# Kernel tuning notes

Hardware: AMD Instinct MI355X
Metric: run time of the kernel (lower is better)

The kernel has to match this reference:

```python
import jax, jax.numpy as jnp
import numpy as np

TEMPERATURE = 0.1

# Constant linear map replacing the nested-loop diagonal masks:
# M[i, j, k] = 1 if i + j == k, shape (10, 10, 19).
_ii, _jj = np.meshgrid(np.arange(10), np.arange(10), indexing='ij')
_M = np.zeros((10, 10, 19), dtype=np.float32)
_M[_ii, _jj, _ii + _jj] = 1.0
DIAG_SUM = jnp.asarray(_M)


def setup_inputs() -> dict:
    key = jax.random.key(0)
    ks = jax.random.split(key, 8)
    B = 16384
    grid = jax.random.normal(ks[0], (B, 4, 28, 28), dtype=jnp.float32)
    # random one-hot program ids
    pid = jax.random.randint(ks[1], (B,), 0, 4)
    program_onehot = jax.nn.one_hot(pid, 4, dtype=jnp.float32)
    W1 = jax.random.normal(ks[2], (784, 256), dtype=jnp.float32) * 0.05
    b1 = jnp.zeros((256,), dtype=jnp.float32)
    W2 = jax.random.normal(ks[3], (256, 10), dtype=jnp.float32) * 0.05
    b2 = jnp.zeros((10,), dtype=jnp.float32)
    Wp = jax.random.normal(ks[4], (4, 16), dtype=jnp.float32) * 0.3
    bp = jnp.zeros((16,), dtype=jnp.float32)
    Wr1 = jax.random.normal(ks[5], (16, 4), dtype=jnp.float32) * 0.3
    br1 = jnp.zeros((4,), dtype=jnp.float32)
    Wr2 = jax.random.normal(ks[6], (16, 4), dtype=jnp.float32) * 0.3
    br2 = jnp.zeros((4,), dtype=jnp.float32)
    return {"grid": grid, "program_onehot": program_onehot,
            "W1": W1, "b1": b1, "W2": W2, "b2": b2,
            "Wp": Wp, "bp": bp, "Wr1": Wr1, "br1": br1,
            "Wr2": Wr2, "br2": br2}


def reference(grid, program_onehot, W1, b1, W2, b2, Wp, bp, Wr1, br1, Wr2, br2):
    B = grid.shape[0]
    # digit_net: 784 -> 256 -> 10 MLP on each of the 4 sub-images
    x = grid.reshape(B * 4, 784)
    h1 = jax.nn.relu(x @ W1 + b1)
    logits = h1 @ W2 + b2                       # (B*4, 10)
    digit_probs = jax.nn.softmax(logits / TEMPERATURE, axis=-1).reshape(B, 4, 10)
    # pointer network
    h = program_onehot @ Wp + bp                 # (B, 16)
    ptr1 = jax.nn.softmax(h @ Wr1 + br1, axis=-1)  # (B, 4)
    ptr2 = jax.nn.softmax(h @ Wr2 + br2, axis=-1)  # (B, 4)
    dist1 = jnp.einsum('bp,bpd->bd', ptr1, digit_probs)  # (B, 10)
    dist2 = jnp.einsum('bp,bpd->bd', ptr2, digit_probs)  # (B, 10)
    outer = dist1[:, :, None] * dist2[:, None, :]         # (B, 10, 10)
    outer_sym = 0.5 * (outer + jnp.swapaxes(outer, 1, 2))
    # diagonal-sum convolution as one contraction against the constant map
    sum_distribution = jnp.einsum('bij,ijk->bk', outer_sym, DIAG_SUM)  # (B, 19)
    return jnp.log(sum_distribution + 1e-10)
```

## Files before the change

### kernel.cpp

```cpp
#include <hip/hip_runtime.h>
#include <hip/hip_bf16.h>

typedef __attribute__((ext_vector_type(8))) short bf16x8;
typedef __attribute__((ext_vector_type(4))) float f32x4;

__device__ __forceinline__ short f2bf(float f) {
    union { float f; unsigned u; } v; v.f = f;
    unsigned r = v.u + 0x7fffu + ((v.u >> 16) & 1u);
    return (short)(r >> 16);
}

#define KP  800
#define LDK 40
#define NKT 25

__global__ void init_kernel(const float* __restrict__ W1, const float* __restrict__ W2,
                            const float* __restrict__ Wp, const float* __restrict__ bp,
                            const float* __restrict__ Wr1, const float* __restrict__ br1,
                            const float* __restrict__ Wr2, const float* __restrict__ br2,
                            short* __restrict__ w1t, short* __restrict__ w2t,
                            float* __restrict__ ptabs)
{
    int tid = blockIdx.x * blockDim.x + threadIdx.x;
    int stride = gridDim.x * blockDim.x;
    for (int i = tid; i < 256 * KP; i += stride) {
        int n = i / KP, k = i - n * KP;
        float v = (k < 784) ? W1[k * 256 + n] : 0.f;
        w1t[i] = f2bf(v);
    }
    for (int i = tid; i < 16 * 256; i += stride) {
        int n = i >> 8, k = i & 255;
        float v = (n < 10) ? W2[k * 10 + n] : 0.f;
        w2t[i] = f2bf(v);
    }
    if (blockIdx.x == 0 && threadIdx.x < 8) {
        int which = threadIdx.x >> 2, p = threadIdx.x & 3;
        const float* Wr = which ? Wr2 : Wr1;
        const float* br = which ? br2 : br1;
        float s[4];
        for (int q = 0; q < 4; q++) {
            float a = br[q];
            for (int j = 0; j < 16; j++) a += (Wp[p * 16 + j] + bp[j]) * Wr[j * 4 + q];
            s[q] = a;
        }
        float m = fmaxf(fmaxf(s[0], s[1]), fmaxf(s[2], s[3]));
        float e[4]; float tot = 0.f;
        for (int q = 0; q < 4; q++) { e[q] = __expf(s[q] - m); tot += e[q]; }
        for (int q = 0; q < 4; q++) ptabs[which * 16 + p * 4 + q] = e[q] / tot;
    }
}

__global__ __launch_bounds__(512, 4) void fused_kernel(
    const float* __restrict__ g_in, const float* __restrict__ onehot,
    const float* __restrict__ b1g, const float* __restrict__ b2g,
    const short* __restrict__ w1t, const short* __restrict__ w2t,
    const float* __restrict__ ptabs, float* __restrict__ out)
{
    __shared__ __align__(16) char lds[78464];
    short* Abuf = (short*)lds;
    short* Bbuf = (short*)(lds + 20480);
    short* h1   = (short*)lds;
    float* probs = (float*)(lds + 67584);
    float* dist1 = (float*)(lds + 75776);
    float* dist2 = (float*)(lds + 77056);

    const int t = threadIdx.x;
    const int lane = t & 63, wave = t >> 6;
    const int l16 = lane & 15, lg = lane >> 4;
    const int wr = wave >> 2, wc = wave & 3;
    const int blk = blockIdx.x;

    const int ar = t >> 2, aq = t & 3;
    const int bn = t >> 1, bh = t & 1;
    const float* gA = g_in + ((long)blk * 128 + ar) * 784 + aq * 8;
    const short* gB = w1t + bn * KP + bh * 16;
    short* awp = Abuf + ar * LDK + aq * 8;
    short* bwp = Bbuf + bn * LDK + bh * 16;

    f32x4 acc[4][4];
    #pragma unroll
    for (int mi = 0; mi < 4; mi++)
        #pragma unroll
        for (int ni = 0; ni < 4; ni++)
            acc[mi][ni] = (f32x4)0.f;

    f32x4 x0, x1; bf16x8 y0, y1;
    auto load_tile = [&](int kt) {
        const int k0 = kt * 32;
        if (k0 + aq * 8 < 784) {
            x0 = *(const f32x4*)(gA + k0);
            x1 = *(const f32x4*)(gA + k0 + 4);
        } else { x0 = (f32x4)0.f; x1 = (f32x4)0.f; }
        y0 = *(const bf16x8*)(gB + k0);
        y1 = *(const bf16x8*)(gB + k0 + 8);
    };
    auto write_tile = [&](int buf) {
        bf16x8 a8;
        a8[0] = f2bf(x0[0]); a8[1] = f2bf(x0[1]); a8[2] = f2bf(x0[2]); a8[3] = f2bf(x0[3]);
        a8[4] = f2bf(x1[0]); a8[5] = f2bf(x1[1]); a8[6] = f2bf(x1[2]); a8[7] = f2bf(x1[3]);
        *(bf16x8*)(awp + buf * (128 * LDK)) = a8;
        *(bf16x8*)(bwp + buf * (256 * LDK)) = y0;
        *(bf16x8*)(bwp + buf * (256 * LDK) + 8) = y1;
    };

    load_tile(0); write_tile(0);
    __syncthreads();
    int cur = 0;
    for (int kt = 0; kt < NKT; kt++) {
        const bool more = (kt + 1 < NKT);
        if (more) load_tile(kt + 1);
        const short* ab = Abuf + cur * (128 * LDK);
        const short* bb = Bbuf + cur * (256 * LDK);
        bf16x8 aF[4], bF[4];
        #pragma unroll
        for (int mi = 0; mi < 4; mi++)
            aF[mi] = *(const bf16x8*)(ab + (wr * 64 + mi * 16 + l16) * LDK + lg * 8);
        #pragma unroll
        for (int ni = 0; ni < 4; ni++)
            bF[ni] = *(const bf16x8*)(bb + (wc * 64 + ni * 16 + l16) * LDK + lg * 8);
        #pragma unroll
        for (int mi = 0; mi < 4; mi++)
            #pragma unroll
            for (int ni = 0; ni < 4; ni++)
                acc[mi][ni] = __builtin_amdgcn_mfma_f32_16x16x32_bf16(aF[mi], bF[ni], acc[mi][ni], 0, 0, 0);
        if (more) write_tile(cur ^ 1);
        __syncthreads();
        cur ^= 1;
    }

    #pragma unroll
    for (int mi = 0; mi < 4; mi++) {
        const int R = wr * 64 + mi * 16 + lg * 4;
        #pragma unroll
        for (int ni = 0; ni < 4; ni++) {
            const int N = wc * 64 + ni * 16 + l16;
            const float bias = b1g[N];
            #pragma unroll
            for (int j = 0; j < 4; j++) {
                float v = acc[mi][ni][j] + bias;
                h1[(R + j) * 264 + N] = f2bf(fmaxf(v, 0.f));
            }
        }
    }
    __syncthreads();

    f32x4 acc2 = (f32x4)0.f;
    const short* h1r = h1 + (wave * 16 + l16) * 264 + lg * 8;
    const short* w2r = w2t + l16 * 256 + lg * 8;
    #pragma unroll
    for (int kk = 0; kk < 8; kk++) {
        bf16x8 a2 = *(const bf16x8*)(h1r + kk * 32);
        bf16x8 b2f = *(const bf16x8*)(w2r + kk * 32);
        acc2 = __builtin_amdgcn_mfma_f32_16x16x32_bf16(a2, b2f, acc2, 0, 0, 0);
    }

    const float b2v = (l16 < 10) ? b2g[l16] : 0.f;
    float pv[4], mx[4];
    #pragma unroll
    for (int j = 0; j < 4; j++) {
        pv[j] = (l16 < 10) ? (acc2[j] + b2v) * 10.f : -1e30f;
        mx[j] = pv[j];
    }
    #pragma unroll
    for (int off = 1; off < 16; off <<= 1)
        #pragma unroll
        for (int j = 0; j < 4; j++)
            mx[j] = fmaxf(mx[j], __shfl_xor(mx[j], off));
    float ex[4], sm[4];
    #pragma unroll
    for (int j = 0; j < 4; j++) { ex[j] = __expf(pv[j] - mx[j]); sm[j] = ex[j]; }
    #pragma unroll
    for (int off = 1; off < 16; off <<= 1)
        #pragma unroll
        for (int j = 0; j < 4; j++)
            sm[j] += __shfl_xor(sm[j], off);
    #pragma unroll
    for (int j = 0; j < 4; j++)
        probs[(wave * 16 + lg * 4 + j) * 16 + l16] = ex[j] / sm[j];
    __syncthreads();

    if (t < 320) {
        int s = t / 10, d = t - s * 10;
        const float* oh = onehot + ((long)blk * 32 + s) * 4;
        int pid = (int)(oh[1] + 2.f * oh[2] + 3.f * oh[3] + 0.5f);
        const float* p1t = ptabs + pid * 4;
        const float* p2t = ptabs + 16 + pid * 4;
        float d1 = 0.f, d2 = 0.f;
        #pragma unroll
        for (int p = 0; p < 4; p++) {
            float pr = probs[(s * 4 + p) * 16 + d];
            d1 += p1t[p] * pr;
            d2 += p2t[p] * pr;
        }
        dist1[s * 10 + d] = d1;
        dist2[s * 10 + d] = d2;
    }
    __syncthreads();

    for (int idx = t; idx < 608; idx += 512) {
        int s = idx / 19, k = idx - s * 19;
        int ilo = k > 9 ? k - 9 : 0;
        int ihi = k < 9 ? k : 9;
        float sum = 0.f;
        for (int i = ilo; i <= ihi; i++)
            sum += dist1[s * 10 + i] * dist2[s * 10 + (k - i)];
        out[((long)blk * 32 + s) * 19 + k] = __logf(sum + 1e-10f);
    }
}

extern "C" void kernel_launch(void* const* d_in, const int* in_sizes, int n_in,
                              void* d_out, int out_size, void* d_ws, size_t ws_size,
                              hipStream_t stream)
{
    const float* grid   = (const float*)d_in[0];
    const float* onehot = (const float*)d_in[1];
    const float* W1  = (const float*)d_in[2];
    const float* b1  = (const float*)d_in[3];
    const float* W2  = (const float*)d_in[4];
    const float* b2  = (const float*)d_in[5];
    const float* Wp  = (const float*)d_in[6];
    const float* bp  = (const float*)d_in[7];
    const float* Wr1 = (const float*)d_in[8];
    const float* br1 = (const float*)d_in[9];
    const float* Wr2 = (const float*)d_in[10];
    const float* br2 = (const float*)d_in[11];
    float* out = (float*)d_out;

    short* w1t = (short*)d_ws;
    short* w2t = w1t + 256 * KP;
    float* ptabs = (float*)(w2t + 16 * 256);

    init_kernel<<<256, 256, 0, stream>>>(W1, W2, Wp, bp, Wr1, br1, Wr2, br2, w1t, w2t, ptabs);

    const int B = in_sizes[1] / 4;
    const int nblk = (B * 4) / 128;
    fused_kernel<<<nblk, 512, 0, stream>>>(grid, onehot, b1, b2, w1t, w2t, ptabs, out);
}
```

Before: 55.91 us.

## Load W1 tiles directly into LDS and deepen the A-operand prefetch pipeline

The W1 operand tiles are now copied straight from global memory into LDS with global_load_lds, so they no longer pass through registers and ds_write. The A (grid) tiles are prefetched two K-steps ahead, using manually unrolled ping-pong buffers with explicit vmcnt/lgkmcnt waits and raw s_barrier. The init kernel now reads W1 in coalesced order when transposing it. In exchange, the B tile in LDS loses its padding (row stride 32), which can cause bank conflicts on fragment reads, and the hand-placed waitcnt values must stay correct.

```diff
diff --git a/kernel.cpp b/kernel.cpp
--- a/kernel.cpp
+++ b/kernel.cpp
@@ -10,9 +10,22 @@
     return (short)(r >> 16);
 }
 
+__device__ __forceinline__ void gl2lds16(const void* g, void* l) {
+    __builtin_amdgcn_global_load_lds(
+        (const __attribute__((address_space(1))) unsigned int*)g,
+        (__attribute__((address_space(3))) unsigned int*)l,
+        16, 0, 0);
+}
+
 #define KP  800
-#define LDK 40
 #define NKT 25
+#define LDKA 40
+
+#define WAITV2 asm volatile("s_waitcnt vmcnt(2)" ::: "memory")
+#define WAITV0 asm volatile("s_waitcnt vmcnt(0)" ::: "memory")
+#define WAITL  asm volatile("s_waitcnt lgkmcnt(0)" ::: "memory")
+#define SBAR   __builtin_amdgcn_s_barrier()
+#define SCHED0 __builtin_amdgcn_sched_barrier(0)
 
 __global__ void init_kernel(const float* __restrict__ W1, const float* __restrict__ W2,
                             const float* __restrict__ Wp, const float* __restrict__ bp,
@@ -23,10 +36,13 @@
 {
     int tid = blockIdx.x * blockDim.x + threadIdx.x;
     int stride = gridDim.x * blockDim.x;
-    for (int i = tid; i < 256 * KP; i += stride) {
-        int n = i / KP, k = i - n * KP;
-        float v = (k < 784) ? W1[k * 256 + n] : 0.f;
-        w1t[i] = f2bf(v);
+    for (int i = tid; i < 784 * 256; i += stride) {
+        int k = i >> 8, n = i & 255;
+        w1t[n * KP + k] = f2bf(W1[i]);
+    }
+    for (int i = tid; i < 256 * 16; i += stride) {
+        int n = i >> 4, k = 784 + (i & 15);
+        w1t[n * KP + k] = 0;
     }
     for (int i = tid; i < 16 * 256; i += stride) {
         int n = i >> 8, k = i & 255;
@@ -71,11 +87,9 @@
     const int blk = blockIdx.x;
 
     const int ar = t >> 2, aq = t & 3;
-    const int bn = t >> 1, bh = t & 1;
     const float* gA = g_in + ((long)blk * 128 + ar) * 784 + aq * 8;
-    const short* gB = w1t + bn * KP + bh * 16;
-    short* awp = Abuf + ar * LDK + aq * 8;
-    short* bwp = Bbuf + bn * LDK + bh * 16;
+    const short* gB = w1t + ar * KP + aq * 8;
+    char* lB = (char*)Bbuf + wave * 1024;
 
     f32x4 acc[4][4];
     #pragma unroll
@@ -84,49 +98,76 @@
         for (int ni = 0; ni < 4; ni++)
             acc[mi][ni] = (f32x4)0.f;
 
-    f32x4 x0, x1; bf16x8 y0, y1;
-    auto load_tile = [&](int kt) {
+    f32x4 xa0, xa1, xb0, xb1;
+
+    auto issueA = [&](int kt, f32x4& x0, f32x4& x1) {
         const int k0 = kt * 32;
         if (k0 + aq * 8 < 784) {
             x0 = *(const f32x4*)(gA + k0);
             x1 = *(const f32x4*)(gA + k0 + 4);
         } else { x0 = (f32x4)0.f; x1 = (f32x4)0.f; }
-        y0 = *(const bf16x8*)(gB + k0);
-        y1 = *(const bf16x8*)(gB + k0 + 8);
-    };
-    auto write_tile = [&](int buf) {
+    };
+    auto issueB = [&](int kt, int buf) {
+        const short* g0 = gB + kt * 32;
+        char* l0 = lB + buf * 16384;
+        gl2lds16(g0, l0);
+        gl2lds16(g0 + 128 * KP, l0 + 8192);
+    };
+    auto writeA = [&](const f32x4& x0, const f32x4& x1, int buf) {
         bf16x8 a8;
         a8[0] = f2bf(x0[0]); a8[1] = f2bf(x0[1]); a8[2] = f2bf(x0[2]); a8[3] = f2bf(x0[3]);
         a8[4] = f2bf(x1[0]); a8[5] = f2bf(x1[1]); a8[6] = f2bf(x1[2]); a8[7] = f2bf(x1[3]);
-        *(bf16x8*)(awp + buf * (128 * LDK)) = a8;
-        *(bf16x8*)(bwp + buf * (256 * LDK)) = y0;
-        *(bf16x8*)(bwp + buf * (256 * LDK) + 8) = y1;
-    };
-
-    load_tile(0); write_tile(0);
-    __syncthreads();
-    int cur = 0;
-    for (int kt = 0; kt < NKT; kt++) {
-        const bool more = (kt + 1 < NKT);
-        if (more) load_tile(kt + 1);
-        const short* ab = Abuf + cur * (128 * LDK);
-        const short* bb = Bbuf + cur * (256 * LDK);
+        *(bf16x8*)(Abuf + buf * (128 * LDKA) + ar * LDKA + aq * 8) = a8;
+    };
+    auto mfmaStep = [&](int buf) {
+        const short* ab = Abuf + buf * (128 * LDKA);
+        const short* bb = Bbuf + buf * (256 * 32);
         bf16x8 aF[4], bF[4];
         #pragma unroll
         for (int mi = 0; mi < 4; mi++)
-            aF[mi] = *(const bf16x8*)(ab + (wr * 64 + mi * 16 + l16) * LDK + lg * 8);
+            aF[mi] = *(const bf16x8*)(ab + (wr * 64 + mi * 16 + l16) * LDKA + lg * 8);
         #pragma unroll
         for (int ni = 0; ni < 4; ni++)
-            bF[ni] = *(const bf16x8*)(bb + (wc * 64 + ni * 16 + l16) * LDK + lg * 8);
+            bF[ni] = *(const bf16x8*)(bb + (wc * 64 + ni * 16 + l16) * 32 + lg * 8);
         #pragma unroll
         for (int mi = 0; mi < 4; mi++)
             #pragma unroll
             for (int ni = 0; ni < 4; ni++)
                 acc[mi][ni] = __builtin_amdgcn_mfma_f32_16x16x32_bf16(aF[mi], bF[ni], acc[mi][ni], 0, 0, 0);
-        if (more) write_tile(cur ^ 1);
-        __syncthreads();
-        cur ^= 1;
-    }
+    };
+
+    issueB(0, 0); SCHED0;
+    issueA(0, xa0, xa1); SCHED0;
+    issueA(1, xb0, xb1); SCHED0;
+    writeA(xa0, xa1, 0);
+    WAITV2; WAITL; SBAR;
+
+    for (int it = 0; it < 11; ++it) {
+        const int kt = it * 2;
+        issueB(kt + 1, 1); SCHED0;
+        issueA(kt + 2, xa0, xa1); SCHED0;
+        mfmaStep(0);
+        writeA(xb0, xb1, 1);
+        WAITV2; WAITL; SBAR;
+        issueB(kt + 2, 0); SCHED0;
+        issueA(kt + 3, xb0, xb1); SCHED0;
+        mfmaStep(1);
+        writeA(xa0, xa1, 0);
+        WAITV2; WAITL; SBAR;
+    }
+    issueB(23, 1); SCHED0;
+    issueA(24, xa0, xa1); SCHED0;
+    mfmaStep(0);
+    writeA(xb0, xb1, 1);
+    WAITV2; WAITL; SBAR;
+
+    issueB(24, 0); SCHED0;
+    mfmaStep(1);
+    writeA(xa0, xa1, 0);
+    WAITV0; WAITL; SBAR;
+
+    mfmaStep(0);
+    WAITL; SBAR;
 
     #pragma unroll
     for (int mi = 0; mi < 4; mi++) {
```

New measurement: 56.82 us. No clear change (+1.6%).

## Halve M tile to 64 rows and restructure GEMM pipeline with decoupled A/B staging

Applied to the files above, without the earlier changes.

Each block now handles 64 rows instead of 128, doubling the grid. The A operand is staged in 128-wide K chunks and the B operand in 32-wide chunks, each double-buffered. The main loop is hand-unrolled with explicit lgkmcnt waits and raw barriers, and init_kernel now reads W1 coalesced when transposing it. The aim is better occupancy and overlap of global loads with MFMA, at the cost of reloading W1 twice as often across blocks, and it relies on hand-placed barriers being correct.

```diff
diff --git a/kernel.cpp b/kernel.cpp
--- a/kernel.cpp
+++ b/kernel.cpp
@@ -10,9 +10,15 @@
     return (short)(r >> 16);
 }
 
-#define KP  800
-#define LDK 40
-#define NKT 25
+#define KP    896
+#define KSTEP 128
+#define LDA   136
+#define LDB   40
+#define ABUFS (64 * LDA)
+#define BBUFS (256 * LDB)
+
+#define WAITL  asm volatile("s_waitcnt lgkmcnt(0)" ::: "memory")
+#define SBAR   __builtin_amdgcn_s_barrier()
 
 __global__ void init_kernel(const float* __restrict__ W1, const float* __restrict__ W2,
                             const float* __restrict__ Wp, const float* __restrict__ bp,
@@ -23,10 +29,13 @@
 {
     int tid = blockIdx.x * blockDim.x + threadIdx.x;
     int stride = gridDim.x * blockDim.x;
-    for (int i = tid; i < 256 * KP; i += stride) {
-        int n = i / KP, k = i - n * KP;
-        float v = (k < 784) ? W1[k * 256 + n] : 0.f;
-        w1t[i] = f2bf(v);
+    for (int i = tid; i < 784 * 256; i += stride) {
+        int k = i >> 8, n = i & 255;
+        w1t[n * KP + k] = f2bf(W1[i]);
+    }
+    for (int i = tid; i < 256 * 112; i += stride) {
+        int n = i / 112, k = 784 + (i % 112);
+        w1t[n * KP + k] = 0;
     }
     for (int i = tid; i < 16 * 256; i += stride) {
         int n = i >> 8, k = i & 255;
@@ -56,13 +65,13 @@
     const short* __restrict__ w1t, const short* __restrict__ w2t,
     const float* __restrict__ ptabs, float* __restrict__ out)
 {
-    __shared__ __align__(16) char lds[78464];
+    __shared__ __align__(16) char lds[79616];
     short* Abuf = (short*)lds;
-    short* Bbuf = (short*)(lds + 20480);
+    short* Bbuf = (short*)(lds + 34816);
     short* h1   = (short*)lds;
-    float* probs = (float*)(lds + 67584);
-    float* dist1 = (float*)(lds + 75776);
-    float* dist2 = (float*)(lds + 77056);
+    float* probs = (float*)(lds + 75776);
+    float* dist1 = (float*)(lds + 78336);
+    float* dist2 = (float*)(lds + 78976);
 
     const int t = threadIdx.x;
     const int lane = t & 63, wave = t >> 6;
@@ -70,67 +79,113 @@
     const int wr = wave >> 2, wc = wave & 3;
     const int blk = blockIdx.x;
 
-    const int ar = t >> 2, aq = t & 3;
+    const int arow = t >> 3, tr = t & 7;
+    const float* gA = g_in + ((long)blk * 64 + arow) * 784 + tr * 16;
     const int bn = t >> 1, bh = t & 1;
-    const float* gA = g_in + ((long)blk * 128 + ar) * 784 + aq * 8;
     const short* gB = w1t + bn * KP + bh * 16;
-    short* awp = Abuf + ar * LDK + aq * 8;
-    short* bwp = Bbuf + bn * LDK + bh * 16;
-
-    f32x4 acc[4][4];
+
+    f32x4 acc[2][4];
     #pragma unroll
-    for (int mi = 0; mi < 4; mi++)
+    for (int mi = 0; mi < 2; mi++)
         #pragma unroll
         for (int ni = 0; ni < 4; ni++)
             acc[mi][ni] = (f32x4)0.f;
 
-    f32x4 x0, x1; bf16x8 y0, y1;
-    auto load_tile = [&](int kt) {
-        const int k0 = kt * 32;
-        if (k0 + aq * 8 < 784) {
-            x0 = *(const f32x4*)(gA + k0);
-            x1 = *(const f32x4*)(gA + k0 + 4);
-        } else { x0 = (f32x4)0.f; x1 = (f32x4)0.f; }
-        y0 = *(const bf16x8*)(gB + k0);
-        y1 = *(const bf16x8*)(gB + k0 + 8);
-    };
-    auto write_tile = [&](int buf) {
-        bf16x8 a8;
-        a8[0] = f2bf(x0[0]); a8[1] = f2bf(x0[1]); a8[2] = f2bf(x0[2]); a8[3] = f2bf(x0[3]);
-        a8[4] = f2bf(x1[0]); a8[5] = f2bf(x1[1]); a8[6] = f2bf(x1[2]); a8[7] = f2bf(x1[3]);
-        *(bf16x8*)(awp + buf * (128 * LDK)) = a8;
-        *(bf16x8*)(bwp + buf * (256 * LDK)) = y0;
-        *(bf16x8*)(bwp + buf * (256 * LDK) + 8) = y1;
-    };
-
-    load_tile(0); write_tile(0);
-    __syncthreads();
-    int cur = 0;
-    for (int kt = 0; kt < NKT; kt++) {
-        const bool more = (kt + 1 < NKT);
-        if (more) load_tile(kt + 1);
-        const short* ab = Abuf + cur * (128 * LDK);
-        const short* bb = Bbuf + cur * (256 * LDK);
-        bf16x8 aF[4], bF[4];
-        #pragma unroll
-        for (int mi = 0; mi < 4; mi++)
-            aF[mi] = *(const bf16x8*)(ab + (wr * 64 + mi * 16 + l16) * LDK + lg * 8);
+    f32x4 xA0, xA1, xA2, xA3;
+    bf16x8 yA0, yA1, yB0, yB1;
+
+    auto issueA = [&](int kt) {
+        const float* p = gA + kt * KSTEP;
+        bool v = (kt < 6) | (tr == 0);
+        if (v) { xA0 = *(const f32x4*)p; xA1 = *(const f32x4*)(p + 4);
+                 xA2 = *(const f32x4*)(p + 8); xA3 = *(const f32x4*)(p + 12); }
+        else   { xA0 = (f32x4)0.f; xA1 = (f32x4)0.f; xA2 = (f32x4)0.f; xA3 = (f32x4)0.f; }
+    };
+    auto writeA = [&](int kt) {
+        bf16x8 a0, a1;
+        a0[0]=f2bf(xA0[0]); a0[1]=f2bf(xA0[1]); a0[2]=f2bf(xA0[2]); a0[3]=f2bf(xA0[3]);
+        a0[4]=f2bf(xA1[0]); a0[5]=f2bf(xA1[1]); a0[6]=f2bf(xA1[2]); a0[7]=f2bf(xA1[3]);
+        a1[0]=f2bf(xA2[0]); a1[1]=f2bf(xA2[1]); a1[2]=f2bf(xA2[2]); a1[3]=f2bf(xA2[3]);
+        a1[4]=f2bf(xA3[0]); a1[5]=f2bf(xA3[1]); a1[6]=f2bf(xA3[2]); a1[7]=f2bf(xA3[3]);
+        short* w = Abuf + (kt & 1) * ABUFS + arow * LDA + tr * 16;
+        *(bf16x8*)w = a0;
+        *(bf16x8*)(w + 8) = a1;
+    };
+    auto issueB0 = [&](int c) {
+        const short* p = gB + c * 32;
+        yA0 = *(const bf16x8*)p; yA1 = *(const bf16x8*)(p + 8);
+    };
+    auto issueB1 = [&](int c) {
+        const short* p = gB + c * 32;
+        yB0 = *(const bf16x8*)p; yB1 = *(const bf16x8*)(p + 8);
+    };
+    auto writeB0 = [&](int c) {
+        short* w = Bbuf + (c & 1) * BBUFS + bn * LDB + bh * 16;
+        *(bf16x8*)w = yA0; *(bf16x8*)(w + 8) = yA1;
+    };
+    auto writeB1 = [&](int c) {
+        short* w = Bbuf + (c & 1) * BBUFS + bn * LDB + bh * 16;
+        *(bf16x8*)w = yB0; *(bf16x8*)(w + 8) = yB1;
+    };
+    auto mfmaSub = [&](int abuf, int bbuf, int s) {
+        const short* ab = Abuf + abuf * ABUFS;
+        const short* bb = Bbuf + bbuf * BBUFS;
+        bf16x8 aF[2], bF[4];
+        #pragma unroll
+        for (int mi = 0; mi < 2; mi++)
+            aF[mi] = *(const bf16x8*)(ab + (wr * 32 + mi * 16 + l16) * LDA + s * 32 + lg * 8);
         #pragma unroll
         for (int ni = 0; ni < 4; ni++)
-            bF[ni] = *(const bf16x8*)(bb + (wc * 64 + ni * 16 + l16) * LDK + lg * 8);
-        #pragma unroll
-        for (int mi = 0; mi < 4; mi++)
+            bF[ni] = *(const bf16x8*)(bb + (wc * 64 + ni * 16 + l16) * LDB + lg * 8);
+        #pragma unroll
+        for (int mi = 0; mi < 2; mi++)
             #pragma unroll
             for (int ni = 0; ni < 4; ni++)
                 acc[mi][ni] = __builtin_amdgcn_mfma_f32_16x16x32_bf16(aF[mi], bF[ni], acc[mi][ni], 0, 0, 0);
-        if (more) write_tile(cur ^ 1);
-        __syncthreads();
-        cur ^= 1;
-    }
+    };
+
+    issueB0(0); issueB1(1); issueA(0);
+    writeB0(0);
+    writeA(0);
+    WAITL; SBAR;
+
+    for (int kt = 0; kt < 6; ++kt) {
+        const int c0 = kt * 4, a = kt & 1;
+        issueB0(c0 + 2); issueA(kt + 1);
+        mfmaSub(a, 0, 0);
+        writeB1(c0 + 1);
+        WAITL; SBAR;
+        issueB1(c0 + 3);
+        mfmaSub(a, 1, 1);
+        writeB0(c0 + 2);
+        WAITL; SBAR;
+        issueB0(c0 + 4);
+        mfmaSub(a, 0, 2);
+        writeB1(c0 + 3);
+        writeA(kt + 1);
+        WAITL; SBAR;
+        issueB1(c0 + 5);
+        mfmaSub(a, 1, 3);
+        writeB0(c0 + 4);
+        WAITL; SBAR;
+    }
+    issueB0(26);
+    mfmaSub(0, 0, 0);
+    writeB1(25);
+    WAITL; SBAR;
+    issueB1(27);
+    mfmaSub(0, 1, 1);
+    writeB0(26);
+    WAITL; SBAR;
+    mfmaSub(0, 0, 2);
+    writeB1(27);
+    WAITL; SBAR;
+    mfmaSub(0, 1, 3);
+    WAITL; SBAR;
 
     #pragma unroll
-    for (int mi = 0; mi < 4; mi++) {
-        const int R = wr * 64 + mi * 16 + lg * 4;
+    for (int mi = 0; mi < 2; mi++) {
+        const int R = wr * 32 + mi * 16 + lg * 4;
         #pragma unroll
         for (int ni = 0; ni < 4; ni++) {
             const int N = wc * 64 + ni * 16 + l16;
@@ -144,51 +199,53 @@
     }
     __syncthreads();
 
-    f32x4 acc2 = (f32x4)0.f;
-    const short* h1r = h1 + (wave * 16 + l16) * 264 + lg * 8;
-    const short* w2r = w2t + l16 * 256 + lg * 8;
-    #pragma unroll
-    for (int kk = 0; kk < 8; kk++) {
-        bf16x8 a2 = *(const bf16x8*)(h1r + kk * 32);
-        bf16x8 b2f = *(const bf16x8*)(w2r + kk * 32);
-        acc2 = __builtin_amdgcn_mfma_f32_16x16x32_bf16(a2, b2f, acc2, 0, 0, 0);
-    }
-
-    const float b2v = (l16 < 10) ? b2g[l16] : 0.f;
-    float pv[4], mx[4];
-    #pragma unroll
-    for (int j = 0; j < 4; j++) {
-        pv[j] = (l16 < 10) ? (acc2[j] + b2v) * 10.f : -1e30f;
-        mx[j] = pv[j];
-    }
-    #pragma unroll
-    for (int off = 1; off < 16; off <<= 1)
-        #pragma unroll
-        for (int j = 0; j < 4; j++)
-            mx[j] = fmaxf(mx[j], __shfl_xor(mx[j], off));
-    float ex[4], sm[4];
-    #pragma unroll
-    for (int j = 0; j < 4; j++) { ex[j] = __expf(pv[j] - mx[j]); sm[j] = ex[j]; }
-    #pragma unroll
-    for (int off = 1; off < 16; off <<= 1)
-        #pragma unroll
-        for (int j = 0; j < 4; j++)
-            sm[j] += __shfl_xor(sm[j], off);
-    #pragma unroll
-    for (int j = 0; j < 4; j++)
-        probs[(wave * 16 + lg * 4 + j) * 16 + l16] = ex[j] / sm[j];
+    if (wave < 4) {
+        f32x4 acc2 = (f32x4)0.f;
+        const short* h1r = h1 + (wave * 16 + l16) * 264 + lg * 8;
+        const short* w2r = w2t + l16 * 256 + lg * 8;
+        #pragma unroll
+        for (int kk = 0; kk < 8; kk++) {
+            bf16x8 a2 = *(const bf16x8*)(h1r + kk * 32);
+            bf16x8 b2f = *(const bf16x8*)(w2r + kk * 32);
+            acc2 = __builtin_amdgcn_mfma_f32_16x16x32_bf16(a2, b2f, acc2, 0, 0, 0);
+        }
+        const float b2v = (l16 < 10) ? b2g[l16] : 0.f;
+        float pv[4], mx[4];
+        #pragma unroll
+        for (int j = 0; j < 4; j++) {
+            pv[j] = (l16 < 10) ? (acc2[j] + b2v) * 10.f : -1e30f;
+            mx[j] = pv[j];
+        }
+        #pragma unroll
+        for (int off = 1; off < 16; off <<= 1)
+            #pragma unroll
+            for (int j = 0; j < 4; j++)
+                mx[j] = fmaxf(mx[j], __shfl_xor(mx[j], off));
+        float ex[4], sm[4];
+        #pragma unroll
+        for (int j = 0; j < 4; j++) { ex[j] = __expf(pv[j] - mx[j]); sm[j] = ex[j]; }
+        #pragma unroll
+        for (int off = 1; off < 16; off <<= 1)
+            #pragma unroll
+            for (int j = 0; j < 4; j++)
+                sm[j] += __shfl_xor(sm[j], off);
+        if (l16 < 10)
+            #pragma unroll
+            for (int j = 0; j < 4; j++)
+                probs[(wave * 16 + lg * 4 + j) * 10 + l16] = ex[j] / sm[j];
+    }
     __syncthreads();
 
-    if (t < 320) {
+    if (t < 160) {
         int s = t / 10, d = t - s * 10;
-        const float* oh = onehot + ((long)blk * 32 + s) * 4;
+        const float* oh = onehot + ((long)blk * 16 + s) * 4;
         int pid = (int)(oh[1] + 2.f * oh[2] + 3.f * oh[3] + 0.5f);
         const float* p1t = ptabs + pid * 4;
         const float* p2t = ptabs + 16 + pid * 4;
         float d1 = 0.f, d2 = 0.f;
         #pragma unroll
         for (int p = 0; p < 4; p++) {
-            float pr = probs[(s * 4 + p) * 16 + d];
+            float pr = probs[(s * 4 + p) * 10 + d];
             d1 += p1t[p] * pr;
             d2 += p2t[p] * pr;
         }
@@ -197,14 +254,14 @@
     }
     __syncthreads();
 
-    for (int idx = t; idx < 608; idx += 512) {
-        int s = idx / 19, k = idx - s * 19;
+    if (t < 304) {
+        int s = t / 19, k = t - s * 19;
         int ilo = k > 9 ? k - 9 : 0;
         int ihi = k < 9 ? k : 9;
         float sum = 0.f;
         for (int i = ilo; i <= ihi; i++)
             sum += dist1[s * 10 + i] * dist2[s * 10 + (k - i)];
-        out[((long)blk * 32 + s) * 19 + k] = __logf(sum + 1e-10f);
+        out[((long)blk * 16 + s) * 19 + k] = __logf(sum + 1e-10f);
     }
 }
 
@@ -233,6 +290,6 @@
     init_kernel<<<256, 256, 0, stream>>>(W1, W2, Wp, bp, Wr1, br1, Wr2, br2, w1t, w2t, ptabs);
 
     const int B = in_sizes[1] / 4;
-    const int nblk = (B * 4) / 128;
+    const int nblk = (B * 4) / 64;
     fused_kernel<<<nblk, 512, 0, stream>>>(grid, onehot, b1, b2, w1t, w2t, ptabs, out);
 }
```

Measured after the change: 76.91 us. +37.6%, slower.

## Restructure MLP GEMM to stream full-K row chunks with W1 read from global

Applied to the files above, without the earlier changes.

Each block now handles 256 rows in 8 chunks of 32 rows. The full 784-wide A row is staged in LDS in bf16 and double-buffered across chunks. Each wave owns 32 output columns and reads its W1 fragments straight from global/L2, no longer staging W1 tiles in LDS. The per-step barriers inside the K loop go away, and the next chunk's loads are software-pipelined against the MFMAs. In exchange, LDS use roughly doubles (occupancy drops to 2 blocks), per-chunk epilogue syncs are added, and W1 is reloaded from L2 by every block for every chunk. The init kernel's W1 transpose is also reworked for coalesced reads.

```diff
diff --git a/kernel.cpp b/kernel.cpp
--- a/kernel.cpp
+++ b/kernel.cpp
@@ -2,6 +2,7 @@
 #include <hip/hip_bf16.h>
 
 typedef __attribute__((ext_vector_type(8))) short bf16x8;
+typedef __attribute__((ext_vector_type(4))) short s16x4;
 typedef __attribute__((ext_vector_type(4))) float f32x4;
 
 __device__ __forceinline__ short f2bf(float f) {
@@ -11,8 +12,8 @@
 }
 
 #define KP  800
-#define LDK 40
-#define NKT 25
+#define LDA 808
+#define LDH 264
 
 __global__ void init_kernel(const float* __restrict__ W1, const float* __restrict__ W2,
                             const float* __restrict__ Wp, const float* __restrict__ bp,
@@ -23,10 +24,13 @@
 {
     int tid = blockIdx.x * blockDim.x + threadIdx.x;
     int stride = gridDim.x * blockDim.x;
-    for (int i = tid; i < 256 * KP; i += stride) {
-        int n = i / KP, k = i - n * KP;
-        float v = (k < 784) ? W1[k * 256 + n] : 0.f;
-        w1t[i] = f2bf(v);
+    for (int i = tid; i < 784 * 256; i += stride) {
+        int k = i >> 8, n = i & 255;
+        w1t[n * KP + k] = f2bf(W1[i]);
+    }
+    for (int i = tid; i < 256 * 16; i += stride) {
+        int n = i >> 4, k = 784 + (i & 15);
+        w1t[n * KP + k] = 0;
     }
     for (int i = tid; i < 16 * 256; i += stride) {
         int n = i >> 8, k = i & 255;
@@ -50,162 +54,196 @@
     }
 }
 
-__global__ __launch_bounds__(512, 4) void fused_kernel(
+__global__ __launch_bounds__(512, 2) void fused_kernel(
     const float* __restrict__ g_in, const float* __restrict__ onehot,
     const float* __restrict__ b1g, const float* __restrict__ b2g,
     const short* __restrict__ w1t, const short* __restrict__ w2t,
     const float* __restrict__ ptabs, float* __restrict__ out)
 {
-    __shared__ __align__(16) char lds[78464];
-    short* Abuf = (short*)lds;
-    short* Bbuf = (short*)(lds + 20480);
-    short* h1   = (short*)lds;
-    float* probs = (float*)(lds + 67584);
-    float* dist1 = (float*)(lds + 75776);
-    float* dist2 = (float*)(lds + 77056);
+    __shared__ __align__(16) char lds[122496];
+    short* Abuf  = (short*)lds;
+    short* h1    = (short*)(lds + 103424);
+    float* probs = (float*)(lds + 120320);
+    float* dist1 = (float*)(lds + 121600);
+    float* dist2 = (float*)(lds + 121920);
+    int*   pids  = (int*)(lds + 122240);
 
     const int t = threadIdx.x;
     const int lane = t & 63, wave = t >> 6;
     const int l16 = lane & 15, lg = lane >> 4;
-    const int wr = wave >> 2, wc = wave & 3;
     const int blk = blockIdx.x;
-
-    const int ar = t >> 2, aq = t & 3;
-    const int bn = t >> 1, bh = t & 1;
-    const float* gA = g_in + ((long)blk * 128 + ar) * 784 + aq * 8;
-    const short* gB = w1t + bn * KP + bh * 16;
-    short* awp = Abuf + ar * LDK + aq * 8;
-    short* bwp = Bbuf + bn * LDK + bh * 16;
-
-    f32x4 acc[4][4];
+    const float* gblock = g_in + (long)blk * 256 * 784;
+
+    if (t < 64) {
+        const float* oh = onehot + ((long)blk * 64 + t) * 4;
+        pids[t] = (int)(oh[1] + 2.f * oh[2] + 3.f * oh[3] + 0.5f);
+    }
+    for (int i = t; i < 2 * 32 * 24; i += 512) {
+        int b = i / 768, rem = i - b * 768;
+        int rr = rem / 24, cc = rem - rr * 24;
+        Abuf[b * 32 * LDA + rr * LDA + 784 + cc] = 0;
+    }
     #pragma unroll
-    for (int mi = 0; mi < 4; mi++)
+    for (int r = 0; r < 13; ++r) {
+        if (r < 12 || t < 128) {
+            int f = r * 2048 + t * 4;
+            f32x4 x = *(const f32x4*)(gblock + f);
+            int row = f / 784, col = f - row * 784;
+            s16x4 a4;
+            a4[0] = f2bf(x[0]); a4[1] = f2bf(x[1]); a4[2] = f2bf(x[2]); a4[3] = f2bf(x[3]);
+            *(s16x4*)(Abuf + row * LDA + col) = a4;
+        }
+    }
+    __syncthreads();
+
+    const short* gw1 = w1t + (wave * 32 + l16) * KP + lg * 8;
+    const float b1v0 = b1g[wave * 32 + l16];
+    const float b1v1 = b1g[wave * 32 + 16 + l16];
+    const float b2v = (l16 < 10) ? b2g[l16] : 0.f;
+
+    #define A_ISSUE(r, xreg) { \
+        if ((r) < 12 || t < 128) { \
+            int f_ = (r) * 2048 + t * 4; \
+            xreg = *(const f32x4*)(gnext + f_); \
+        } }
+    #define A_WRITE(r, xreg) { \
+        if ((r) < 12 || t < 128) { \
+            int f_ = (r) * 2048 + t * 4; \
+            int row_ = f_ / 784, col_ = f_ - row_ * 784; \
+            s16x4 a4_; \
+            a4_[0] = f2bf(xreg[0]); a4_[1] = f2bf(xreg[1]); \
+            a4_[2] = f2bf(xreg[2]); a4_[3] = f2bf(xreg[3]); \
+            *(s16x4*)(Awr + row_ * LDA + col_) = a4_; \
+        } }
+    #define BF_ISSUE(s1, dst) { \
+        dst[0] = *(const bf16x8*)(gw1 + (s1) * 32); \
+        dst[1] = *(const bf16x8*)(gw1 + 16 * KP + (s1) * 32); }
+    #define AF_ISSUE(s1, dst) { \
+        dst[0] = *(const bf16x8*)(Ard + l16 * LDA + (s1) * 32 + lg * 8); \
+        dst[1] = *(const bf16x8*)(Ard + (16 + l16) * LDA + (s1) * 32 + lg * 8); }
+    #define DO_MFMA(af, bf) { \
+        acc00 = __builtin_amdgcn_mfma_f32_16x16x32_bf16(af[0], bf[0], acc00, 0, 0, 0); \
+        acc01 = __builtin_amdgcn_mfma_f32_16x16x32_bf16(af[0], bf[1], acc01, 0, 0, 0); \
+        acc10 = __builtin_amdgcn_mfma_f32_16x16x32_bf16(af[1], bf[0], acc10, 0, 0, 0); \
+        acc11 = __builtin_amdgcn_mfma_f32_16x16x32_bf16(af[1], bf[1], acc11, 0, 0, 0); }
+
+    for (int c = 0; c < 8; ++c) {
+        const short* Ard = Abuf + (c & 1) * (32 * LDA);
+        short* Awr = Abuf + ((c + 1) & 1) * (32 * LDA);
+        const float* gnext = gblock + (c + 1) * 25088;
+        const bool stage = (c < 7);
+
+        f32x4 acc00 = (f32x4)0.f, acc01 = (f32x4)0.f, acc10 = (f32x4)0.f, acc11 = (f32x4)0.f;
+        bf16x8 bfE[2], bfO[2], afE[2], afO[2];
+        f32x4 xE, xO;
+
+        BF_ISSUE(0, bfE);
+        AF_ISSUE(0, afE);
+
         #pragma unroll
-        for (int ni = 0; ni < 4; ni++)
-            acc[mi][ni] = (f32x4)0.f;
-
-    f32x4 x0, x1; bf16x8 y0, y1;
-    auto load_tile = [&](int kt) {
-        const int k0 = kt * 32;
-        if (k0 + aq * 8 < 784) {
-            x0 = *(const f32x4*)(gA + k0);
-            x1 = *(const f32x4*)(gA + k0 + 4);
-        } else { x0 = (f32x4)0.f; x1 = (f32x4)0.f; }
-        y0 = *(const bf16x8*)(gB + k0);
-        y1 = *(const bf16x8*)(gB + k0 + 8);
-    };
-    auto write_tile = [&](int buf) {
-        bf16x8 a8;
-        a8[0] = f2bf(x0[0]); a8[1] = f2bf(x0[1]); a8[2] = f2bf(x0[2]); a8[3] = f2bf(x0[3]);
-        a8[4] = f2bf(x1[0]); a8[5] = f2bf(x1[1]); a8[6] = f2bf(x1[2]); a8[7] = f2bf(x1[3]);
-        *(bf16x8*)(awp + buf * (128 * LDK)) = a8;
-        *(bf16x8*)(bwp + buf * (256 * LDK)) = y0;
-        *(bf16x8*)(bwp + buf * (256 * LDK) + 8) = y1;
-    };
-
-    load_tile(0); write_tile(0);
-    __syncthreads();
-    int cur = 0;
-    for (int kt = 0; kt < NKT; kt++) {
-        const bool more = (kt + 1 < NKT);
-        if (more) load_tile(kt + 1);
-        const short* ab = Abuf + cur * (128 * LDK);
-        const short* bb = Bbuf + cur * (256 * LDK);
-        bf16x8 aF[4], bF[4];
+        for (int s = 0; s < 25; ++s) {
+            if (stage) {
+                if ((s & 1) == 0 && s >= 2 && s <= 22) {
+                    const int r = s / 2 - 1;
+                    if (r & 1) { A_WRITE(r, xO); } else { A_WRITE(r, xE); }
+                }
+                if (s == 23) { A_WRITE(11, xO); }
+                if (s == 24) { A_WRITE(12, xE); }
+            }
+            if (s < 24) {
+                if ((s + 1) & 1) { BF_ISSUE(s + 1, bfO); AF_ISSUE(s + 1, afO); }
+                else             { BF_ISSUE(s + 1, bfE); AF_ISSUE(s + 1, afE); }
+            }
+            if (stage) {
+                if ((s & 1) == 0 && s <= 20) {
+                    const int r = s / 2;
+                    if (r & 1) { A_ISSUE(r, xO); } else { A_ISSUE(r, xE); }
+                }
+                if (s == 21) { A_ISSUE(11, xO); }
+                if (s == 22) { A_ISSUE(12, xE); }
+            }
+            if (s & 1) { DO_MFMA(afO, bfO); } else { DO_MFMA(afE, bfE); }
+        }
+        __syncthreads();
+
         #pragma unroll
-        for (int mi = 0; mi < 4; mi++)
-            aF[mi] = *(const bf16x8*)(ab + (wr * 64 + mi * 16 + l16) * LDK + lg * 8);
-        #pragma unroll
-        for (int ni = 0; ni < 4; ni++)
-            bF[ni] = *(const bf16x8*)(bb + (wc * 64 + ni * 16 + l16) * LDK + lg * 8);
-        #pragma unroll
-        for (int mi = 0; mi < 4; mi++)
-            #pragma unroll
-            for (int ni = 0; ni < 4; ni++)
-                acc[mi][ni] = __builtin_amdgcn_mfma_f32_16x16x32_bf16(aF[mi], bF[ni], acc[mi][ni], 0, 0, 0);
-        if (more) write_tile(cur ^ 1);
-        __syncthreads();
-        cur ^= 1;
-    }
-
-    #pragma unroll
-    for (int mi = 0; mi < 4; mi++) {
-        const int R = wr * 64 + mi * 16 + lg * 4;
-        #pragma unroll
-        for (int ni = 0; ni < 4; ni++) {
-            const int N = wc * 64 + ni * 16 + l16;
-            const float bias = b1g[N];
+        for (int j = 0; j < 4; ++j) {
+            int r0 = lg * 4 + j, r1 = 16 + lg * 4 + j;
+            h1[r0 * LDH + wave * 32 + l16]      = f2bf(fmaxf(acc00[j] + b1v0, 0.f));
+            h1[r0 * LDH + wave * 32 + 16 + l16] = f2bf(fmaxf(acc01[j] + b1v1, 0.f));
+            h1[r1 * LDH + wave * 32 + l16]      = f2bf(fmaxf(acc10[j] + b1v0, 0.f));
+            h1[r1 * LDH + wave * 32 + 16 + l16] = f2bf(fmaxf(acc11[j] + b1v1, 0.f));
+        }
+        __syncthreads();
+
+        if (wave < 2) {
+            f32x4 acc2 = (f32x4)0.f;
+            const short* h1r = h1 + (wave * 16 + l16) * LDH + lg * 8;
+            const short* w2r = w2t + l16 * 256 + lg * 8;
+            #pragma unroll
+            for (int kk = 0; kk < 8; kk++) {
+                bf16x8 a2 = *(const bf16x8*)(h1r + kk * 32);
+                bf16x8 b2f = *(const bf16x8*)(w2r + kk * 32);
+                acc2 = __builtin_amdgcn_mfma_f32_16x16x32_bf16(a2, b2f, acc2, 0, 0, 0);
+            }
+            float pv[4], mx[4];
             #pragma unroll
             for (int j = 0; j < 4; j++) {
-                float v = acc[mi][ni][j] + bias;
-                h1[(R + j) * 264 + N] = f2bf(fmaxf(v, 0.f));
-            }
-        }
-    }
-    __syncthreads();
-
-    f32x4 acc2 = (f32x4)0.f;
-    const short* h1r = h1 + (wave * 16 + l16) * 264 + lg * 8;
-    const short* w2r = w2t + l16 * 256 + lg * 8;
-    #pragma unroll
-    for (int kk = 0; kk < 8; kk++) {
-        bf16x8 a2 = *(const bf16x8*)(h1r + kk * 32);
-        bf16x8 b2f = *(const bf16x8*)(w2r + kk * 32);
-        acc2 = __builtin_amdgcn_mfma_f32_16x16x32_bf16(a2, b2f, acc2, 0, 0, 0);
-    }
-
-    const float b2v = (l16 < 10) ? b2g[l16] : 0.f;
-    float pv[4], mx[4];
-    #pragma unroll
-    for (int j = 0; j < 4; j++) {
-        pv[j] = (l16 < 10) ? (acc2[j] + b2v) * 10.f : -1e30f;
-        mx[j] = pv[j];
-    }
-    #pragma unroll
-    for (int off = 1; off < 16; off <<= 1)
-        #pragma unroll
-        for (int j = 0; j < 4; j++)
-            mx[j] = fmaxf(mx[j], __shfl_xor(mx[j], off));
-    float ex[4], sm[4];
-    #pragma unroll
-    for (int j = 0; j < 4; j++) { ex[j] = __expf(pv[j] - mx[j]); sm[j] = ex[j]; }
-    #pragma unroll
-    for (int off = 1; off < 16; off <<= 1)
-        #pragma unroll
-        for (int j = 0; j < 4; j++)
-            sm[j] += __shfl_xor(sm[j], off);
-    #pragma unroll
-    for (int j = 0; j < 4; j++)
-        probs[(wave * 16 + lg * 4 + j) * 16 + l16] = ex[j] / sm[j];
-    __syncthreads();
-
-    if (t < 320) {
-        int s = t / 10, d = t - s * 10;
-        const float* oh = onehot + ((long)blk * 32 + s) * 4;
-        int pid = (int)(oh[1] + 2.f * oh[2] + 3.f * oh[3] + 0.5f);
-        const float* p1t = ptabs + pid * 4;
-        const float* p2t = ptabs + 16 + pid * 4;
-        float d1 = 0.f, d2 = 0.f;
-        #pragma unroll
-        for (int p = 0; p < 4; p++) {
-            float pr = probs[(s * 4 + p) * 16 + d];
-            d1 += p1t[p] * pr;
-            d2 += p2t[p] * pr;
-        }
-        dist1[s * 10 + d] = d1;
-        dist2[s * 10 + d] = d2;
-    }
-    __syncthreads();
-
-    for (int idx = t; idx < 608; idx += 512) {
-        int s = idx / 19, k = idx - s * 19;
-        int ilo = k > 9 ? k - 9 : 0;
-        int ihi = k < 9 ? k : 9;
-        float sum = 0.f;
-        for (int i = ilo; i <= ihi; i++)
-            sum += dist1[s * 10 + i] * dist2[s * 10 + (k - i)];
-        out[((long)blk * 32 + s) * 19 + k] = __logf(sum + 1e-10f);
-    }
+                pv[j] = (l16 < 10) ? (acc2[j] + b2v) * 10.f : -1e30f;
+                mx[j] = pv[j];
+            }
+            #pragma unroll
+            for (int off = 1; off < 16; off <<= 1)
+                #pragma unroll
+                for (int j = 0; j < 4; j++)
+                    mx[j] = fmaxf(mx[j], __shfl_xor(mx[j], off));
+            float ex[4], sm[4];
+            #pragma unroll
+            for (int j = 0; j < 4; j++) { ex[j] = __expf(pv[j] - mx[j]); sm[j] = ex[j]; }
+            #pragma unroll
+            for (int off = 1; off < 16; off <<= 1)
+                #pragma unroll
+                for (int j = 0; j < 4; j++)
+                    sm[j] += __shfl_xor(sm[j], off);
+            if (l16 < 10)
+                #pragma unroll
+                for (int j = 0; j < 4; j++)
+                    probs[(wave * 16 + lg * 4 + j) * 10 + l16] = ex[j] / sm[j];
+        }
+        __syncthreads();
+
+        if (t < 80) {
+            int s = t / 10, d = t - s * 10;
+            int pid = pids[c * 8 + s];
+            const float* p1t = ptabs + pid * 4;
+            const float* p2t = ptabs + 16 + pid * 4;
+            float d1 = 0.f, d2 = 0.f;
+            #pragma unroll
+            for (int p = 0; p < 4; p++) {
+                float pr = probs[(s * 4 + p) * 10 + d];
+                d1 += p1t[p] * pr;
+                d2 += p2t[p] * pr;
+            }
+            dist1[s * 10 + d] = d1;
+            dist2[s * 10 + d] = d2;
+        }
+        __syncthreads();
+
+        if (t < 152) {
+            int s = t / 19, k = t - s * 19;
+            int ilo = k > 9 ? k - 9 : 0;
+            int ihi = k < 9 ? k : 9;
+            float sum = 0.f;
+            for (int i = ilo; i <= ihi; i++)
+                sum += dist1[s * 10 + i] * dist2[s * 10 + (k - i)];
+            out[((long)blk * 64 + c * 8 + s) * 19 + k] = __logf(sum + 1e-10f);
+        }
+    }
+    #undef A_ISSUE
+    #undef A_WRITE
+    #undef BF_ISSUE
+    #undef AF_ISSUE
+    #undef DO_MFMA
 }
 
 extern "C" void kernel_launch(void* const* d_in, const int* in_sizes, int n_in,
@@ -233,6 +271,6 @@
     init_kernel<<<256, 256, 0, stream>>>(W1, W2, Wp, bp, Wr1, br1, Wr2, br2, w1t, w2t, ptabs);
 
     const int B = in_sizes[1] / 4;
-    const int nblk = (B * 4) / 128;
+    const int nblk = (B * 4) / 256;
     fused_kernel<<<nblk, 512, 0, stream>>>(grid, onehot, b1, b2, w1t, w2t, ptabs, out);
 }
```

Result: slower. 160.7 us (+187.4%).
